# Kernel optimization log

Measured on AMD Instinct MI355X. Metric: run time of the kernel, lower is better.

The kernel has to match this reference:

```python
import jax, jax.numpy as jnp
import numpy as np

B, S, E = 8, 2048, 1024

def setup_inputs() -> dict:
    key = jax.random.key(0)
    ks = jax.random.split(key, 9)
    def xavier(k, shape):
        fan_in, fan_out = shape[1], shape[0]
        lim = (6.0 / (fan_in + fan_out)) ** 0.5
        return jax.random.uniform(k, shape, jnp.float32, -lim, lim)
    return {
        "queries": jax.random.normal(ks[0], (B, S, E), jnp.float32),
        "keys":    jax.random.normal(ks[1], (B, S, E), jnp.float32),
        "values":  jax.random.normal(ks[2], (B, S, E), jnp.float32),
        "Wq": xavier(ks[3], (E, E)), "bq": jnp.zeros((E,), jnp.float32),
        "Wk": xavier(ks[4], (E, E)), "bk": jnp.zeros((E,), jnp.float32),
        "Wv": xavier(ks[5], (E, E)), "bv": jnp.zeros((E,), jnp.float32),
    }

def reference(queries, keys, values, Wq, bq, Wk, bk, Wv, bv):
    # torch Linear: x @ W.T + b
    q = jnp.einsum('bse,fe->bsf', queries, Wq) + bq
    k = jnp.einsum('bse,fe->bsf', keys, Wk) + bk
    v = jnp.einsum('bse,fe->bsf', values, Wv) + bv
    d = q.shape[-1]
    scores = jnp.einsum('bqe,bke->bqk', q, k) / jnp.sqrt(jnp.float32(d))
    attn = jax.nn.softmax(scores, axis=-1)
    # dropout is identity at inference
    out = jnp.einsum('bqk,bke->bqe', attn, v)
    return jnp.squeeze(out, axis=1) if out.shape[1] == 1 else out
```

## Files before the change

### kernel.cpp

```cpp
#include <hip/hip_runtime.h>
#include <stdint.h>

typedef float f32x4 __attribute__((ext_vector_type(4)));
typedef __bf16 bf16x8 __attribute__((ext_vector_type(8)));

__device__ __forceinline__ uint16_t f2bf(float f) {
    uint32_t x = __builtin_bit_cast(uint32_t, f);
    uint32_t lsb = (x >> 16) & 1u;
    return (uint16_t)((x + 0x7fffu + lsb) >> 16);
}
__device__ __forceinline__ float bf2f(uint32_t u) {
    return __builtin_bit_cast(float, u << 16);
}

__device__ __forceinline__ void gload16(const uint16_t* g, uint16_t* l) {
    __builtin_amdgcn_global_load_lds(
        (const __attribute__((address_space(1))) uint32_t*)g,
        (__attribute__((address_space(3))) uint32_t*)l,
        16, 0, 0);
}

__global__ __launch_bounds__(256) void zero_f32(float* __restrict__ p, int n) {
    int i = blockIdx.x * 256 + threadIdx.x;
    if (i < n) p[i] = 0.f;
}

__global__ __launch_bounds__(256) void cvt_f32_bf16(
    const float* __restrict__ src, uint16_t* __restrict__ dst, int n8)
{
    int idx = blockIdx.x * 256 + threadIdx.x;
    int stride = gridDim.x * 256;
    for (int i = idx; i < n8; i += stride) {
        const float4* s = (const float4*)src + 2 * (size_t)i;
        float4 a = s[0], b = s[1];
        uint4 o;
        o.x = (uint32_t)f2bf(a.x) | ((uint32_t)f2bf(a.y) << 16);
        o.y = (uint32_t)f2bf(a.z) | ((uint32_t)f2bf(a.w) << 16);
        o.z = (uint32_t)f2bf(b.x) | ((uint32_t)f2bf(b.y) << 16);
        o.w = (uint32_t)f2bf(b.z) | ((uint32_t)f2bf(b.w) << 16);
        ((uint4*)dst)[i] = o;
    }
}

template<typename TO, int BIAS_MODE, int EPI>
__global__ __launch_bounds__(256, 4) void gemm_bf16(
    const uint16_t* __restrict__ A, const uint16_t* __restrict__ Bm,
    const float* __restrict__ bias, float* __restrict__ lsum, TO* __restrict__ D,
    int lda, int ldb, int ldd, int K, int ntn,
    long long sA, long long sB, long long sD, float scale)
{
    __shared__ uint16_t Ash[128 * 32];
    __shared__ uint16_t Bsh[128 * 32];

    int bid = blockIdx.x;
    const int nx = gridDim.x;
    bid = (bid & 7) * (nx >> 3) + (bid >> 3);
    const int tm = bid / ntn;
    const int tn = bid % ntn;
    const int bz = blockIdx.y;
    A  += (size_t)bz * sA;
    Bm += (size_t)bz * sB;
    D  += (size_t)bz * sD;
    float* lz = (EPI != 0) ? (lsum + (size_t)bz * 2048) : nullptr;

    const int m0 = tm * 128, n0 = tn * 128;
    const int t = threadIdx.x;
    const int wid = t >> 6, lane = t & 63;
    const int wm = wid >> 1, wn = wid & 1;
    const int r16 = lane & 15, g = lane >> 4;

    const int lr = lane >> 2, l4 = lane & 3;
    const int c0 = 2 * wid;
    const int arow0 = c0 * 16 + lr;
    const int acol  = l4 * 8;

    f32x4 acc[4][4];
#pragma unroll
    for (int i = 0; i < 4; ++i)
#pragma unroll
        for (int j = 0; j < 4; ++j)
            acc[i][j] = (f32x4){0.f, 0.f, 0.f, 0.f};

    const uint16_t* aS = A  + (size_t)(m0 + arow0) * lda + acol;
    const uint16_t* bS = Bm + (size_t)(n0 + arow0) * ldb + acol;
    uint16_t* aD0 = &Ash[c0 * 512];
    uint16_t* aD1 = &Ash[c0 * 512 + 512];
    uint16_t* bD0 = &Bsh[c0 * 512];
    uint16_t* bD1 = &Bsh[c0 * 512 + 512];

    for (int k0 = 0; k0 < K; k0 += 32) {
        __syncthreads();
        gload16(aS + k0, aD0);
        gload16(aS + k0 + (size_t)16 * lda, aD1);
        gload16(bS + k0, bD0);
        gload16(bS + k0 + (size_t)16 * ldb, bD1);
        __syncthreads();

        uint4 af[4], bf[4];
#pragma unroll
        for (int i = 0; i < 4; ++i)
            af[i] = *(const uint4*)&Ash[(wm * 64 + i * 16 + r16) * 32 + g * 8];
#pragma unroll
        for (int j = 0; j < 4; ++j)
            bf[j] = *(const uint4*)&Bsh[(wn * 64 + j * 16 + r16) * 32 + g * 8];

#pragma unroll
        for (int i = 0; i < 4; ++i)
#pragma unroll
            for (int j = 0; j < 4; ++j)
                acc[i][j] = __builtin_amdgcn_mfma_f32_16x16x32_bf16(
                    __builtin_bit_cast(bf16x8, af[i]),
                    __builtin_bit_cast(bf16x8, bf[j]),
                    acc[i][j], 0, 0, 0);
    }

#pragma unroll
    for (int i = 0; i < 4; ++i) {
        const int grow0 = m0 + wm * 64 + i * 16 + g * 4;
        float rs[4] = {0.f, 0.f, 0.f, 0.f};
        float invl[4];
        if constexpr (EPI == 2) {
#pragma unroll
            for (int r = 0; r < 4; ++r) invl[r] = 1.0f / lz[grow0 + r];
        }
#pragma unroll
        for (int j = 0; j < 4; ++j) {
            const int gcol = n0 + wn * 64 + j * 16 + r16;
            float bcol = (BIAS_MODE == 1) ? bias[gcol] : 0.f;
#pragma unroll
            for (int r = 0; r < 4; ++r) {
                float v = acc[i][j][r];
                float bb = (BIAS_MODE == 1) ? bcol : ((BIAS_MODE == 2) ? bias[grow0 + r] : 0.f);
                v = (v + bb) * scale;
                if constexpr (EPI == 0) {
                    if constexpr (sizeof(TO) == 2)
                        ((uint16_t*)D)[(size_t)(grow0 + r) * ldd + gcol] = f2bf(v);
                    else
                        ((float*)D)[(size_t)(grow0 + r) * ldd + gcol] = v;
                } else if constexpr (EPI == 1) {
                    float e = __expf(v);
                    uint16_t h = f2bf(e);
                    ((uint16_t*)D)[(size_t)(grow0 + r) * ldd + gcol] = h;
                    rs[r] += bf2f(h);
                } else {
                    ((float*)D)[(size_t)(grow0 + r) * ldd + gcol] = v * invl[r];
                }
            }
        }
        if constexpr (EPI == 1) {
#pragma unroll
            for (int r = 0; r < 4; ++r) {
                float s = rs[r];
                s += __shfl_xor(s, 1);
                s += __shfl_xor(s, 2);
                s += __shfl_xor(s, 4);
                s += __shfl_xor(s, 8);
                if ((lane & 15) == 0) atomicAdd(&lz[grow0 + r], s);
            }
        }
    }
}

extern "C" void kernel_launch(void* const* d_in, const int* in_sizes, int n_in,
                              void* d_out, int out_size, void* d_ws, size_t ws_size,
                              hipStream_t stream)
{
    const float* q_in = (const float*)d_in[0];
    const float* k_in = (const float*)d_in[1];
    const float* v_in = (const float*)d_in[2];
    const float* Wq   = (const float*)d_in[3];
    const float* bq   = (const float*)d_in[4];
    const float* Wk   = (const float*)d_in[5];
    const float* bk   = (const float*)d_in[6];
    const float* Wv   = (const float*)d_in[7];
    const float* bv   = (const float*)d_in[8];

    const size_t MS = (size_t)16384 * 1024;
    const size_t WS = (size_t)1024 * 1024;
    const size_t SS = (size_t)8 * 2048 * 2048;
    size_t needed = (3 * MS + SS) * sizeof(uint16_t) + 16384 * sizeof(float);
    if (ws_size < needed) return;

    uint16_t* Qb = (uint16_t*)d_ws;
    uint16_t* Kb = Qb + MS;
    uint16_t* VT = Kb + MS;
    uint16_t* Sc = VT + MS;
    float*    lrow = (float*)(Sc + SS);

    uint16_t* Xv  = Sc;
    uint16_t* Wqb = Sc + MS;
    uint16_t* Wkb = Wqb + WS;
    uint16_t* Wvb = Wkb + WS;
    uint16_t* Xq  = (uint16_t*)d_out;
    uint16_t* Xk  = Xq + MS;

    dim3 blk(256);

    zero_f32<<<dim3(64), blk, 0, stream>>>(lrow, 16384);

    cvt_f32_bf16<<<dim3(2048), blk, 0, stream>>>(q_in, Xq, (int)(MS / 8));
    cvt_f32_bf16<<<dim3(2048), blk, 0, stream>>>(k_in, Xk, (int)(MS / 8));
    cvt_f32_bf16<<<dim3(2048), blk, 0, stream>>>(v_in, Xv, (int)(MS / 8));
    cvt_f32_bf16<<<dim3(256),  blk, 0, stream>>>(Wq, Wqb, (int)(WS / 8));
    cvt_f32_bf16<<<dim3(256),  blk, 0, stream>>>(Wk, Wkb, (int)(WS / 8));
    cvt_f32_bf16<<<dim3(256),  blk, 0, stream>>>(Wv, Wvb, (int)(WS / 8));

    gemm_bf16<uint16_t, 1, 0><<<dim3(128 * 8, 1), blk, 0, stream>>>(
        Xq, Wqb, bq, nullptr, Qb, 1024, 1024, 1024, 1024, 8, 0, 0, 0, 0.03125f);
    gemm_bf16<uint16_t, 1, 0><<<dim3(128 * 8, 1), blk, 0, stream>>>(
        Xk, Wkb, bk, nullptr, Kb, 1024, 1024, 1024, 1024, 8, 0, 0, 0, 1.0f);
    gemm_bf16<uint16_t, 2, 0><<<dim3(8 * 16, 8), blk, 0, stream>>>(
        Wvb, Xv, bv, nullptr, VT, 1024, 1024, 2048, 1024, 16,
        0, (long long)2048 * 1024, (long long)1024 * 2048, 1.0f);
    gemm_bf16<uint16_t, 0, 1><<<dim3(16 * 16, 8), blk, 0, stream>>>(
        Qb, Kb, nullptr, lrow, Sc, 1024, 1024, 2048, 1024, 16,
        (long long)2048 * 1024, (long long)2048 * 1024, (long long)2048 * 2048, 1.0f);
    gemm_bf16<float, 0, 2><<<dim3(16 * 8, 8), blk, 0, stream>>>(
        Sc, VT, nullptr, lrow, (float*)d_out, 2048, 2048, 1024, 2048, 8,
        (long long)2048 * 2048, (long long)1024 * 2048, (long long)2048 * 1024, 1.0f);
}
```

Baseline: 576.0 us.

## Use 256x256 GEMM tiles with triple-buffered LDS, swizzle, and merged conversions

Replaces the 128x128 single-buffered GEMM with a 512-thread, 256x256-tile kernel. It uses a three-slot LDS ring fed by async global-to-LDS loads two tiles ahead, an XOR swizzle to avoid bank conflicts, and setprio around the MFMA bursts. The goal is more data reuse per byte loaded and load latency hidden behind compute instead of a full sync every k-step. The six conversion launches are merged into two by indexing tensors with blockIdx.y. Larger tiles mean fewer blocks (256 or fewer per GEMM), which may underfill the GPU. The prefetch also wraps around and issues redundant loads at the tail.

New measurement: 568.6 us. No clear change (-1.3%).

```diff
diff --git a/kernel.cpp b/kernel.cpp
--- a/kernel.cpp
+++ b/kernel.cpp
@@ -13,7 +13,7 @@
     return __builtin_bit_cast(float, u << 16);
 }
 
-__device__ __forceinline__ void gload16(const uint16_t* g, uint16_t* l) {
+__device__ __forceinline__ void gload16(const uint16_t* g, const uint8_t* l) {
     __builtin_amdgcn_global_load_lds(
         (const __attribute__((address_space(1))) uint32_t*)g,
         (__attribute__((address_space(3))) uint32_t*)l,
@@ -25,9 +25,12 @@
     if (i < n) p[i] = 0.f;
 }
 
-__global__ __launch_bounds__(256) void cvt_f32_bf16(
-    const float* __restrict__ src, uint16_t* __restrict__ dst, int n8)
+__global__ __launch_bounds__(256) void cvt3_f32_bf16(
+    const float* __restrict__ s0, const float* __restrict__ s1, const float* __restrict__ s2,
+    uint16_t* __restrict__ d0, uint16_t* __restrict__ d1, uint16_t* __restrict__ d2, int n8)
 {
+    const float* src = (blockIdx.y == 0) ? s0 : (blockIdx.y == 1) ? s1 : s2;
+    uint16_t*   dst = (blockIdx.y == 0) ? d0 : (blockIdx.y == 1) ? d1 : d2;
     int idx = blockIdx.x * 256 + threadIdx.x;
     int stride = gridDim.x * 256;
     for (int i = idx; i < n8; i += stride) {
@@ -43,80 +46,109 @@
 }
 
 template<typename TO, int BIAS_MODE, int EPI>
-__global__ __launch_bounds__(256, 4) void gemm_bf16(
+__global__ __launch_bounds__(512, 2) void gemm256(
     const uint16_t* __restrict__ A, const uint16_t* __restrict__ Bm,
     const float* __restrict__ bias, float* __restrict__ lsum, TO* __restrict__ D,
     int lda, int ldb, int ldd, int K, int ntn,
     long long sA, long long sB, long long sD, float scale)
 {
-    __shared__ uint16_t Ash[128 * 32];
-    __shared__ uint16_t Bsh[128 * 32];
+    __shared__ uint4 ldsq[6144];
+    uint8_t* ldsb = (uint8_t*)ldsq;
 
     int bid = blockIdx.x;
     const int nx = gridDim.x;
     bid = (bid & 7) * (nx >> 3) + (bid >> 3);
-    const int tm = bid / ntn;
-    const int tn = bid % ntn;
+    const int tm = bid / ntn, tn = bid % ntn;
     const int bz = blockIdx.y;
     A  += (size_t)bz * sA;
     Bm += (size_t)bz * sB;
     D  += (size_t)bz * sD;
     float* lz = (EPI != 0) ? (lsum + (size_t)bz * 2048) : nullptr;
 
-    const int m0 = tm * 128, n0 = tn * 128;
+    const int m0 = tm * 256, n0 = tn * 256;
     const int t = threadIdx.x;
     const int wid = t >> 6, lane = t & 63;
-    const int wm = wid >> 1, wn = wid & 1;
+    const int wm = wid >> 2, wn = wid & 3;
     const int r16 = lane & 15, g = lane >> 4;
 
-    const int lr = lane >> 2, l4 = lane & 3;
+    const int lco = r16 * 64 + ((g ^ ((r16 >> 1) & 3)) << 4);
+
+    const int sslot = (lane & 3) ^ ((lane >> 3) & 3);
     const int c0 = 2 * wid;
-    const int arow0 = c0 * 16 + lr;
-    const int acol  = l4 * 8;
-
-    f32x4 acc[4][4];
-#pragma unroll
-    for (int i = 0; i < 4; ++i)
+    const int gr0 = c0 * 16 + (lane >> 2);
+    const uint16_t* aS0 = A  + (size_t)(m0 + gr0) * lda + sslot * 8;
+    const uint16_t* aS1 = A  + (size_t)(m0 + gr0 + 16) * lda + sslot * 8;
+    const uint16_t* bS0 = Bm + (size_t)(n0 + gr0) * ldb + sslot * 8;
+    const uint16_t* bS1 = Bm + (size_t)(n0 + gr0 + 16) * ldb + sslot * 8;
+    const int dA0 = c0 * 1024, dA1 = dA0 + 1024;
+
+#define STAGE_A(sl, kk) do { uint8_t* _b = ldsb + (sl) * 32768; \
+    gload16(aS0 + (kk), _b + dA0); gload16(aS1 + (kk), _b + dA1); } while (0)
+#define STAGE_B(sl, kk) do { uint8_t* _b = ldsb + (sl) * 32768 + 16384; \
+    gload16(bS0 + (kk), _b + dA0); gload16(bS1 + (kk), _b + dA1); } while (0)
+
+    f32x4 acc[8][4];
+#pragma unroll
+    for (int i = 0; i < 8; ++i)
 #pragma unroll
         for (int j = 0; j < 4; ++j)
             acc[i][j] = (f32x4){0.f, 0.f, 0.f, 0.f};
 
-    const uint16_t* aS = A  + (size_t)(m0 + arow0) * lda + acol;
-    const uint16_t* bS = Bm + (size_t)(n0 + arow0) * ldb + acol;
-    uint16_t* aD0 = &Ash[c0 * 512];
-    uint16_t* aD1 = &Ash[c0 * 512 + 512];
-    uint16_t* bD0 = &Bsh[c0 * 512];
-    uint16_t* bD1 = &Bsh[c0 * 512 + 512];
-
-    for (int k0 = 0; k0 < K; k0 += 32) {
-        __syncthreads();
-        gload16(aS + k0, aD0);
-        gload16(aS + k0 + (size_t)16 * lda, aD1);
-        gload16(bS + k0, bD0);
-        gload16(bS + k0 + (size_t)16 * ldb, bD1);
-        __syncthreads();
-
-        uint4 af[4], bf[4];
-#pragma unroll
-        for (int i = 0; i < 4; ++i)
-            af[i] = *(const uint4*)&Ash[(wm * 64 + i * 16 + r16) * 32 + g * 8];
-#pragma unroll
-        for (int j = 0; j < 4; ++j)
-            bf[j] = *(const uint4*)&Bsh[(wn * 64 + j * 16 + r16) * 32 + g * 8];
-
-#pragma unroll
-        for (int i = 0; i < 4; ++i)
-#pragma unroll
-            for (int j = 0; j < 4; ++j)
-                acc[i][j] = __builtin_amdgcn_mfma_f32_16x16x32_bf16(
-                    __builtin_bit_cast(bf16x8, af[i]),
-                    __builtin_bit_cast(bf16x8, bf[j]),
-                    acc[i][j], 0, 0, 0);
+    const int NT = K >> 5;
+    STAGE_A(0, 0); STAGE_B(0, 0);
+    STAGE_A(1, 32); STAGE_B(1, 32);
+
+    int s_cur = 0;
+    for (int tt = 0; tt < NT; ++tt) {
+        int s2 = s_cur + 2; if (s2 >= 3) s2 -= 3;
+        int t2 = tt + 2; if (t2 >= NT) t2 -= NT;
+        const int kk2 = t2 << 5;
+
+        asm volatile("s_waitcnt vmcnt(4)" ::: "memory");
+        __builtin_amdgcn_s_barrier();
+        asm volatile("" ::: "memory");
+
+        const uint8_t* Ab = ldsb + s_cur * 32768 + wm * 8192;
+        const uint8_t* Bb = ldsb + s_cur * 32768 + 16384 + wn * 4096;
+
+        STAGE_A(s2, kk2);
+        uint4 af[8], bfr[4];
+#pragma unroll
+        for (int m = 0; m < 8; ++m)
+            af[m] = *(const uint4*)(Ab + m * 1024 + lco);
+        bfr[0] = *(const uint4*)(Bb + lco);
+        bfr[1] = *(const uint4*)(Bb + 1024 + lco);
+        __builtin_amdgcn_s_setprio(1);
+#pragma unroll
+        for (int m = 0; m < 8; ++m) {
+            acc[m][0] = __builtin_amdgcn_mfma_f32_16x16x32_bf16(
+                __builtin_bit_cast(bf16x8, af[m]), __builtin_bit_cast(bf16x8, bfr[0]), acc[m][0], 0, 0, 0);
+            acc[m][1] = __builtin_amdgcn_mfma_f32_16x16x32_bf16(
+                __builtin_bit_cast(bf16x8, af[m]), __builtin_bit_cast(bf16x8, bfr[1]), acc[m][1], 0, 0, 0);
+        }
+        __builtin_amdgcn_s_setprio(0);
+
+        STAGE_B(s2, kk2);
+        bfr[2] = *(const uint4*)(Bb + 2048 + lco);
+        bfr[3] = *(const uint4*)(Bb + 3072 + lco);
+        __builtin_amdgcn_s_setprio(1);
+#pragma unroll
+        for (int m = 0; m < 8; ++m) {
+            acc[m][2] = __builtin_amdgcn_mfma_f32_16x16x32_bf16(
+                __builtin_bit_cast(bf16x8, af[m]), __builtin_bit_cast(bf16x8, bfr[2]), acc[m][2], 0, 0, 0);
+            acc[m][3] = __builtin_amdgcn_mfma_f32_16x16x32_bf16(
+                __builtin_bit_cast(bf16x8, af[m]), __builtin_bit_cast(bf16x8, bfr[3]), acc[m][3], 0, 0, 0);
+        }
+        __builtin_amdgcn_s_setprio(0);
+
+        s_cur += 1; if (s_cur >= 3) s_cur = 0;
     }
-
-#pragma unroll
-    for (int i = 0; i < 4; ++i) {
-        const int grow0 = m0 + wm * 64 + i * 16 + g * 4;
+#undef STAGE_A
+#undef STAGE_B
+
+#pragma unroll
+    for (int mf = 0; mf < 8; ++mf) {
+        const int grow0 = m0 + wm * 128 + mf * 16 + g * 4;
         float rs[4] = {0.f, 0.f, 0.f, 0.f};
         float invl[4];
         if constexpr (EPI == 2) {
@@ -124,12 +156,12 @@
             for (int r = 0; r < 4; ++r) invl[r] = 1.0f / lz[grow0 + r];
         }
 #pragma unroll
-        for (int j = 0; j < 4; ++j) {
-            const int gcol = n0 + wn * 64 + j * 16 + r16;
+        for (int nf = 0; nf < 4; ++nf) {
+            const int gcol = n0 + wn * 64 + nf * 16 + r16;
             float bcol = (BIAS_MODE == 1) ? bias[gcol] : 0.f;
 #pragma unroll
             for (int r = 0; r < 4; ++r) {
-                float v = acc[i][j][r];
+                float v = acc[mf][nf][r];
                 float bb = (BIAS_MODE == 1) ? bcol : ((BIAS_MODE == 2) ? bias[grow0 + r] : 0.f);
                 v = (v + bb) * scale;
                 if constexpr (EPI == 0) {
@@ -195,27 +227,26 @@
     uint16_t* Xk  = Xq + MS;
 
     dim3 blk(256);
+    dim3 blk5(512);
 
     zero_f32<<<dim3(64), blk, 0, stream>>>(lrow, 16384);
 
-    cvt_f32_bf16<<<dim3(2048), blk, 0, stream>>>(q_in, Xq, (int)(MS / 8));
-    cvt_f32_bf16<<<dim3(2048), blk, 0, stream>>>(k_in, Xk, (int)(MS / 8));
-    cvt_f32_bf16<<<dim3(2048), blk, 0, stream>>>(v_in, Xv, (int)(MS / 8));
-    cvt_f32_bf16<<<dim3(256),  blk, 0, stream>>>(Wq, Wqb, (int)(WS / 8));
-    cvt_f32_bf16<<<dim3(256),  blk, 0, stream>>>(Wk, Wkb, (int)(WS / 8));
-    cvt_f32_bf16<<<dim3(256),  blk, 0, stream>>>(Wv, Wvb, (int)(WS / 8));
-
-    gemm_bf16<uint16_t, 1, 0><<<dim3(128 * 8, 1), blk, 0, stream>>>(
-        Xq, Wqb, bq, nullptr, Qb, 1024, 1024, 1024, 1024, 8, 0, 0, 0, 0.03125f);
-    gemm_bf16<uint16_t, 1, 0><<<dim3(128 * 8, 1), blk, 0, stream>>>(
-        Xk, Wkb, bk, nullptr, Kb, 1024, 1024, 1024, 1024, 8, 0, 0, 0, 1.0f);
-    gemm_bf16<uint16_t, 2, 0><<<dim3(8 * 16, 8), blk, 0, stream>>>(
-        Wvb, Xv, bv, nullptr, VT, 1024, 1024, 2048, 1024, 16,
+    cvt3_f32_bf16<<<dim3(1024, 3), blk, 0, stream>>>(
+        q_in, k_in, v_in, Xq, Xk, Xv, (int)(MS / 8));
+    cvt3_f32_bf16<<<dim3(128, 3), blk, 0, stream>>>(
+        Wq, Wk, Wv, Wqb, Wkb, Wvb, (int)(WS / 8));
+
+    gemm256<uint16_t, 1, 0><<<dim3(256, 1), blk5, 0, stream>>>(
+        Xq, Wqb, bq, nullptr, Qb, 1024, 1024, 1024, 1024, 4, 0, 0, 0, 0.03125f);
+    gemm256<uint16_t, 1, 0><<<dim3(256, 1), blk5, 0, stream>>>(
+        Xk, Wkb, bk, nullptr, Kb, 1024, 1024, 1024, 1024, 4, 0, 0, 0, 1.0f);
+    gemm256<uint16_t, 2, 0><<<dim3(32, 8), blk5, 0, stream>>>(
+        Wvb, Xv, bv, nullptr, VT, 1024, 1024, 2048, 1024, 8,
         0, (long long)2048 * 1024, (long long)1024 * 2048, 1.0f);
-    gemm_bf16<uint16_t, 0, 1><<<dim3(16 * 16, 8), blk, 0, stream>>>(
-        Qb, Kb, nullptr, lrow, Sc, 1024, 1024, 2048, 1024, 16,
+    gemm256<uint16_t, 0, 1><<<dim3(64, 8), blk5, 0, stream>>>(
+        Qb, Kb, nullptr, lrow, Sc, 1024, 1024, 2048, 1024, 8,
         (long long)2048 * 1024, (long long)2048 * 1024, (long long)2048 * 2048, 1.0f);
-    gemm_bf16<float, 0, 2><<<dim3(16 * 8, 8), blk, 0, stream>>>(
-        Sc, VT, nullptr, lrow, (float*)d_out, 2048, 2048, 1024, 2048, 8,
+    gemm256<float, 0, 2><<<dim3(32, 8), blk5, 0, stream>>>(
+        Sc, VT, nullptr, lrow, (float*)d_out, 2048, 2048, 1024, 2048, 4,
         (long long)2048 * 2048, (long long)1024 * 2048, (long long)2048 * 1024, 1.0f);
 }
```
